# Optimization experiments

Hardware: AMD Instinct MI355X
Metric: run time of the kernel (lower is better)

The kernel has to match this reference:

```python
import jax, jax.numpy as jnp
import numpy as np

OBS, ACT, HID, P, B = 128, 32, 256, 64, 4096
EPS = 1e-5


def _block(x, W, b, g, be, act=True):
    # x: [B, P, Din]; W: [P, Din, Dout]; b/g/be: [P, Dout]
    y = jnp.einsum('bpi,pio->bpo', x, W) + b
    # GroupNorm with one group per sub-policy: normalize over Dout per (b, p)
    mu = jnp.mean(y, axis=-1, keepdims=True)
    var = jnp.var(y, axis=-1, keepdims=True)
    y = (y - mu) * jax.lax.rsqrt(var + EPS) * g + be
    return jax.nn.elu(y) if act else y


def setup_inputs() -> dict:
    key = jax.random.key(0)
    ks = jax.random.split(key, 17)
    s = 0.05
    return {
        'observation': jax.random.normal(ks[0], (B, OBS), dtype=jnp.float32),
        'W1': jax.random.normal(ks[1], (P, OBS, HID), dtype=jnp.float32) * s,
        'b1': jax.random.normal(ks[2], (P, HID), dtype=jnp.float32) * s,
        'g1': jnp.ones((P, HID), dtype=jnp.float32),
        'be1': jnp.zeros((P, HID), dtype=jnp.float32),
        'W2': jax.random.normal(ks[3], (P, HID, HID), dtype=jnp.float32) * s,
        'b2': jax.random.normal(ks[4], (P, HID), dtype=jnp.float32) * s,
        'g2': jnp.ones((P, HID), dtype=jnp.float32),
        'be2': jnp.zeros((P, HID), dtype=jnp.float32),
        'W3': jax.random.normal(ks[5], (P, HID, HID), dtype=jnp.float32) * s,
        'b3': jax.random.normal(ks[6], (P, HID), dtype=jnp.float32) * s,
        'g3': jnp.ones((P, HID), dtype=jnp.float32),
        'be3': jnp.zeros((P, HID), dtype=jnp.float32),
        'W4': jax.random.normal(ks[7], (P, HID, ACT), dtype=jnp.float32) * s,
        'b4': jax.random.normal(ks[8], (P, ACT), dtype=jnp.float32) * s,
        'g4': jnp.ones((P, ACT), dtype=jnp.float32),
        'be4': jnp.zeros((P, ACT), dtype=jnp.float32),
    }


def reference(observation, W1, b1, g1, be1, W2, b2, g2, be2,
              W3, b3, g3, be3, W4, b4, g4, be4):
    # broadcast observation to each sub-policy: [B, P, OBS]
    x = jnp.broadcast_to(observation[:, None, :], (observation.shape[0], P, OBS))
    x = _block(x, W1, b1, g1, be1, act=True)
    x = _block(x, W2, b2, g2, be2, act=True)
    x = _block(x, W3, b3, g3, be3, act=True)
    x = _block(x, W4, b4, g4, be4, act=False)
    return x  # [B, P, ACT] action logits
```

## Files before the change

### kernel.cpp

```cpp
#include <hip/hip_runtime.h>

#define B_    4096
#define P_    64
#define OBS_  128
#define HID_  256
#define ACTD_ 32

typedef __attribute__((ext_vector_type(8)))  __bf16 bf16x8;
typedef __attribute__((ext_vector_type(2)))  __bf16 bf16x2_t;
typedef __attribute__((ext_vector_type(4)))  float  f32x4;
typedef __attribute__((ext_vector_type(16))) float  f32x16;

#define XSTRIDE 264

#define WS1 0L
#define WS2 2097152L
#define WS3 6291456L
#define WS4 10485760L

#if defined(__has_builtin)
#if __has_builtin(__builtin_amdgcn_cvt_pk_bf16_f32)
#define HAVE_CVT_PK_BF16 1
#endif
#endif
#ifndef HAVE_CVT_PK_BF16
#define HAVE_CVT_PK_BF16 0
#endif

__device__ __forceinline__ unsigned short f2bf(float x) {
    unsigned u = __builtin_bit_cast(unsigned, x);
    u = (u + 0x7fffu + ((u >> 16) & 1u)) >> 16;
    return (unsigned short)u;
}

__device__ __forceinline__ unsigned pack_bf16_rne(float a, float b) {
#if HAVE_CVT_PK_BF16
    bf16x2_t p = __builtin_amdgcn_cvt_pk_bf16_f32(a, b);
    return __builtin_bit_cast(unsigned, p);
#else
    unsigned ua = __builtin_bit_cast(unsigned, a);
    unsigned ub = __builtin_bit_cast(unsigned, b);
    ua = ua + 0x7fffu + ((ua >> 16) & 1u);
    ub = ub + 0x7fffu + ((ub >> 16) & 1u);
    return __builtin_amdgcn_perm(ub, ua, 0x07060302u);
#endif
}

__device__ __forceinline__ float elu_asm(float v) {
    float r;
    asm volatile(
        "v_mul_f32 %0, 0x3fb8aa3b, %1\n\t"
        "v_exp_f32 %0, %0\n\t"
        "s_nop 1\n\t"
        "v_add_f32 %0, -1.0, %0\n\t"
        "v_cmp_lt_f32 vcc, 0, %1\n\t"
        "v_cndmask_b32 %0, %0, %1, vcc"
        : "=&v"(r) : "v"(v) : "vcc");
    return r;
}

template<int K, int N, bool PERM>
__device__ __forceinline__ void prep_body(const float* __restrict__ W,
                                          unsigned short* __restrict__ out,
                                          int b, int t)
{
    constexpr int CH = K / 32;
    int tid  = b * 256 + t;
    int n    = tid % N;
    int rest = tid / N;
    int u    = rest % 4;
    rest    /= 4;
    int c    = rest % CH;
    int p    = rest / CH;
    unsigned short tmp[8];
#pragma unroll
    for (int j = 0; j < 8; ++j) {
        int sk = c * 32 + u * 8 + j;
        int k  = PERM ? ((sk & ~63) | ((sk & 1) << 5) | ((sk >> 1) & 31)) : sk;
        tmp[j] = f2bf(W[((long)(p * K + k)) * N + n]);
    }
    unsigned short* dst = out + ((((long)(p * CH + c) * 4 + u) * N + n) * 8);
    *reinterpret_cast<uint4*>(dst) = *reinterpret_cast<const uint4*>(tmp);
}

extern "C" __global__ __launch_bounds__(256)
void prep_all(const float* __restrict__ W1, const float* __restrict__ W2,
              const float* __restrict__ W3, const float* __restrict__ W4,
              unsigned short* __restrict__ ws)
{
    int b = blockIdx.x, t = threadIdx.x;
    if      (b < 1024) prep_body<128, 256, false>(W1, ws + WS1, b,        t);
    else if (b < 3072) prep_body<256, 256, true >(W2, ws + WS2, b - 1024, t);
    else if (b < 5120) prep_body<256, 256, true >(W3, ws + WS3, b - 3072, t);
    else               prep_body<256, 32,  true >(W4, ws + WS4, b - 5120, t);
}

__device__ __forceinline__ void stage(char* lds, const char* src, int nbytes, int tid)
{
    const int lnoff = (tid & 63) * 16;
    const int off   = (tid >> 6) * 1024 + lnoff;
    for (int i = off; i < nbytes; i += 4096) {
        __builtin_amdgcn_global_load_lds(
            (const __attribute__((address_space(1))) unsigned int*)(const void*)(src + i),
            (__attribute__((address_space(3))) unsigned int*)(void*)(lds + (i - lnoff)),
            16, 0, 0);
    }
}

template<int KCH>
__device__ __forceinline__ void layer256(
    unsigned short* __restrict__ X,
    char* __restrict__ Wb0, char* __restrict__ Wb1,
    const char* __restrict__ wsrc,
    const char* __restrict__ nsrc, int nbytes,
    const float* __restrict__ bp, const float* __restrict__ gp, const float* __restrict__ bep,
    float2* __restrict__ part, float2* __restrict__ stats,
    int tid, bool elu)
{
    const int w  = tid >> 6;
    const int l5 = tid & 31;
    const int h  = (tid & 63) >> 5;

    f32x16 acc[2][2];
#pragma unroll
    for (int rt = 0; rt < 2; ++rt)
#pragma unroll
        for (int ct = 0; ct < 2; ++ct)
#pragma unroll
            for (int r = 0; r < 16; ++r) acc[rt][ct][r] = 0.f;

#pragma unroll
    for (int c = 0; c < KCH; ++c) {
        const char* nx = (c + 1 < KCH) ? (wsrc + (long)(c + 1) * 8192) : nsrc;
        int nb         = (c + 1 < KCH) ? 8192 : nbytes;
        stage((c & 1) ? Wb0 : Wb1, nx, nb, tid);

        const char* wc = (c & 1) ? Wb1 : Wb0;
        const int k0 = c * 16 + h * 8;
        bf16x8 a0 = *(const bf16x8*)(X + l5 * XSTRIDE + k0);
        bf16x8 a1 = *(const bf16x8*)(X + (32 + l5) * XSTRIDE + k0);
        const char* bb = wc + h * 4096;
        bf16x8 b0 = *(const bf16x8*)(bb + (w * 64 + l5) * 16);
        bf16x8 b1 = *(const bf16x8*)(bb + (w * 64 + 32 + l5) * 16);
        acc[0][0] = __builtin_amdgcn_mfma_f32_32x32x16_bf16(a0, b0, acc[0][0], 0, 0, 0);
        acc[1][0] = __builtin_amdgcn_mfma_f32_32x32x16_bf16(a1, b0, acc[1][0], 0, 0, 0);
        acc[0][1] = __builtin_amdgcn_mfma_f32_32x32x16_bf16(a0, b1, acc[0][1], 0, 0, 0);
        acc[1][1] = __builtin_amdgcn_mfma_f32_32x32x16_bf16(a1, b1, acc[1][1], 0, 0, 0);
        __syncthreads();
    }

    const int n0 = w * 64 + l5, n1 = n0 + 32;
    const int pos = w * 64 + 2 * l5;
    const float bb0 = bp[n0], bb1 = bp[n1];
#pragma unroll
    for (int rt = 0; rt < 2; ++rt)
#pragma unroll
        for (int r = 0; r < 16; ++r) { acc[rt][0][r] += bb0; acc[rt][1][r] += bb1; }

#pragma unroll
    for (int rt = 0; rt < 2; ++rt)
#pragma unroll
        for (int r = 0; r < 16; ++r) {
            const int row = rt * 32 + (r & 3) + 8 * (r >> 2) + 4 * h;
            *reinterpret_cast<unsigned*>(X + row * XSTRIDE + pos) =
                pack_bf16_rne(acc[rt][0][r], acc[rt][1][r]);
        }

    {
        const int lane = tid & 63;
        float s = 0.f, s2 = 0.f;
#pragma unroll
        for (int j8 = 0; j8 < 8; ++j8) {
            bf16x8 v8 = *(const bf16x8*)(X + lane * XSTRIDE + w * 64 + j8 * 8);
#pragma unroll
            for (int e = 0; e < 8; ++e) { float v = (float)v8[e]; s += v; s2 = fmaf(v, v, s2); }
        }
        part[lane * 4 + w] = make_float2(s, s2);
    }
    __syncthreads();
    if (w == 0) {
        const int lane = tid & 63;
        float2 p0 = part[lane * 4 + 0], p1 = part[lane * 4 + 1];
        float2 p2 = part[lane * 4 + 2], p3 = part[lane * 4 + 3];
        float s  = p0.x + p1.x + p2.x + p3.x;
        float s2 = p0.y + p1.y + p2.y + p3.y;
        float mu  = s * (1.f / 256.f);
        float var = s2 * (1.f / 256.f) - mu * mu;
        stats[lane] = make_float2(mu, rsqrtf(var + 1e-5f));
    }
    __syncthreads();

    const float g0 = gp[n0], g1 = gp[n1], be0 = bep[n0], be1 = bep[n1];
#pragma unroll
    for (int rt = 0; rt < 2; ++rt)
#pragma unroll
        for (int r = 0; r < 16; ++r) {
            const int row = rt * 32 + (r & 3) + 8 * (r >> 2) + 4 * h;
            float2 st = stats[row];
            float v0 = (acc[rt][0][r] - st.x) * st.y * g0 + be0;
            float v1 = (acc[rt][1][r] - st.x) * st.y * g1 + be1;
            if (elu) { v0 = elu_asm(v0); v1 = elu_asm(v1); }
            *reinterpret_cast<unsigned*>(X + row * XSTRIDE + pos) = pack_bf16_rne(v0, v1);
        }
    __syncthreads();
}

__device__ __forceinline__ void layer32(
    const unsigned short* __restrict__ X,
    char* __restrict__ Wb0, char* __restrict__ Wb1,
    const char* __restrict__ wsrc,
    const float* __restrict__ bp, const float* __restrict__ gp, const float* __restrict__ bep,
    float* __restrict__ outg, int bbase, int p, int tid)
{
    const int w = tid >> 6, lane = tid & 63, ln = lane & 15, quad = lane >> 4;
    f32x4 acc[2];
#pragma unroll
    for (int nt = 0; nt < 2; ++nt)
#pragma unroll
        for (int r = 0; r < 4; ++r) acc[nt][r] = 0.f;

#pragma unroll
    for (int c = 0; c < 8; ++c) {
        if (c < 7) stage((c & 1) ? Wb0 : Wb1, wsrc + (long)(c + 1) * 2048, 2048, tid);
        const char* wc = (c & 1) ? Wb1 : Wb0;
        bf16x8 a  = *(const bf16x8*)(X + (16 * w + ln) * XSTRIDE + c * 32 + quad * 8);
        bf16x8 b0 = *(const bf16x8*)(wc + quad * 512 + ln * 16);
        bf16x8 b1 = *(const bf16x8*)(wc + quad * 512 + (16 + ln) * 16);
        acc[0] = __builtin_amdgcn_mfma_f32_16x16x32_bf16(a, b0, acc[0], 0, 0, 0);
        acc[1] = __builtin_amdgcn_mfma_f32_16x16x32_bf16(a, b1, acc[1], 0, 0, 0);
        __syncthreads();
    }

    const float bb0 = bp[ln], bb1 = bp[16 + ln];
    const float g0 = gp[ln], g1 = gp[16 + ln], be0 = bep[ln], be1 = bep[16 + ln];
#pragma unroll
    for (int r = 0; r < 4; ++r) {
        float y0 = acc[0][r] + bb0, y1 = acc[1][r] + bb1;
        float s = y0 + y1, s2 = y0 * y0 + y1 * y1;
        s += __shfl_xor(s, 1);  s2 += __shfl_xor(s2, 1);
        s += __shfl_xor(s, 2);  s2 += __shfl_xor(s2, 2);
        s += __shfl_xor(s, 4);  s2 += __shfl_xor(s2, 4);
        s += __shfl_xor(s, 8);  s2 += __shfl_xor(s2, 8);
        float mu  = s * (1.f / 32.f);
        float var = s2 * (1.f / 32.f) - mu * mu;
        float rs  = rsqrtf(var + 1e-5f);
        const int row = bbase + 16 * w + quad * 4 + r;
        float* o = outg + ((long)row * P_ + p) * ACTD_;
        o[ln]      = (y0 - mu) * rs * g0 + be0;
        o[16 + ln] = (y1 - mu) * rs * g1 + be1;
    }
}

extern "C" __global__ void __launch_bounds__(256, 3)
policy_fused(const float* __restrict__ obs,
             const unsigned short* __restrict__ wbf,
             const float* __restrict__ b1, const float* __restrict__ g1, const float* __restrict__ be1,
             const float* __restrict__ b2, const float* __restrict__ g2, const float* __restrict__ be2,
             const float* __restrict__ b3, const float* __restrict__ g3, const float* __restrict__ be3,
             const float* __restrict__ b4, const float* __restrict__ g4, const float* __restrict__ be4,
             float* __restrict__ out)
{
    __shared__ __align__(16) unsigned short X[64 * XSTRIDE];
    __shared__ __align__(16) char Wbuf0[8192];
    __shared__ __align__(16) char Wbuf1[8192];
    __shared__ float2 part[64 * 4];
    __shared__ float2 stats[64];

    const int tid = threadIdx.x;
    const int bx  = blockIdx.x;
    const int p     = ((bx & 7) << 3) | ((bx >> 3) & 7);
    const int bbase = (bx >> 6) * 64;

    const char* ws1 = (const char*)(wbf + WS1 + (long)p * (128 * 256));
    const char* ws2 = (const char*)(wbf + WS2 + (long)p * (256 * 256));
    const char* ws3 = (const char*)(wbf + WS3 + (long)p * (256 * 256));
    const char* ws4 = (const char*)(wbf + WS4 + (long)p * (256 * 32));

    stage(Wbuf0, ws1, 8192, tid);

    for (int idx = tid; idx < 64 * 32; idx += 256) {
        int row = idx >> 5, c4 = idx & 31;
        float4 v = *reinterpret_cast<const float4*>(obs + (long)(bbase + row) * OBS_ + c4 * 4);
        uint2 pk;
        pk.x = pack_bf16_rne(v.x, v.y);
        pk.y = pack_bf16_rne(v.z, v.w);
        *reinterpret_cast<uint2*>(X + row * XSTRIDE + c4 * 4) = pk;
    }
    __syncthreads();

    layer256<8>(X, Wbuf0, Wbuf1, ws1, ws2, 8192,
                b1 + p * 256, g1 + p * 256, be1 + p * 256, part, stats, tid, true);
    layer256<16>(X, Wbuf0, Wbuf1, ws2, ws3, 8192,
                 b2 + p * 256, g2 + p * 256, be2 + p * 256, part, stats, tid, true);
    layer256<16>(X, Wbuf0, Wbuf1, ws3, ws4, 2048,
                 b3 + p * 256, g3 + p * 256, be3 + p * 256, part, stats, tid, true);
    layer32(X, Wbuf0, Wbuf1, ws4,
            b4 + p * 32, g4 + p * 32, be4 + p * 32, out, bbase, p, tid);
}

extern "C" void kernel_launch(void* const* d_in, const int* in_sizes, int n_in,
                              void* d_out, int out_size, void* d_ws, size_t ws_size,
                              hipStream_t stream)
{
    const float* obs = (const float*)d_in[0];
    const float* W1  = (const float*)d_in[1];
    const float* b1  = (const float*)d_in[2];
    const float* g1  = (const float*)d_in[3];
    const float* be1 = (const float*)d_in[4];
    const float* W2  = (const float*)d_in[5];
    const float* b2  = (const float*)d_in[6];
    const float* g2  = (const float*)d_in[7];
    const float* be2 = (const float*)d_in[8];
    const float* W3  = (const float*)d_in[9];
    const float* b3  = (const float*)d_in[10];
    const float* g3  = (const float*)d_in[11];
    const float* be3 = (const float*)d_in[12];
    const float* W4  = (const float*)d_in[13];
    const float* b4  = (const float*)d_in[14];
    const float* g4  = (const float*)d_in[15];
    const float* be4 = (const float*)d_in[16];
    float* out = (float*)d_out;
    unsigned short* ws = (unsigned short*)d_ws;

    hipLaunchKernelGGL(prep_all, dim3(5376), dim3(256), 0, stream, W1, W2, W3, W4, ws);

    hipLaunchKernelGGL(policy_fused, dim3(4096), dim3(256), 0, stream,
                       obs, ws,
                       b1, g1, be1, b2, g2, be2, b3, g3, be3, b4, g4, be4, out);
}
```

Before: 314.2 us.

## Load weight fragments directly from global memory instead of LDS double-buffering

Removes the LDS staging of weight chunks via global_load_lds with double buffers and per-chunk barriers. Each lane now reads its bf16 weight fragments straight from global (L2-cached) memory inside the fully unrolled K loop. This frees 16KB of LDS per block and drops many __syncthreads, which allows the occupancy hint to rise from 3 to 4 blocks per CU. The cost is that every wave fetches weights from global memory without LDS sharing, so performance now depends on L2 hit rates and on how well the compiler schedules loads ahead of the MFMAs.

```diff
diff --git a/kernel.cpp b/kernel.cpp
--- a/kernel.cpp
+++ b/kernel.cpp
@@ -95,24 +95,10 @@
     else               prep_body<256, 32,  true >(W4, ws + WS4, b - 5120, t);
 }
 
-__device__ __forceinline__ void stage(char* lds, const char* src, int nbytes, int tid)
-{
-    const int lnoff = (tid & 63) * 16;
-    const int off   = (tid >> 6) * 1024 + lnoff;
-    for (int i = off; i < nbytes; i += 4096) {
-        __builtin_amdgcn_global_load_lds(
-            (const __attribute__((address_space(1))) unsigned int*)(const void*)(src + i),
-            (__attribute__((address_space(3))) unsigned int*)(void*)(lds + (i - lnoff)),
-            16, 0, 0);
-    }
-}
-
 template<int KCH>
 __device__ __forceinline__ void layer256(
     unsigned short* __restrict__ X,
-    char* __restrict__ Wb0, char* __restrict__ Wb1,
     const char* __restrict__ wsrc,
-    const char* __restrict__ nsrc, int nbytes,
     const float* __restrict__ bp, const float* __restrict__ gp, const float* __restrict__ bep,
     float2* __restrict__ part, float2* __restrict__ stats,
     int tid, bool elu)
@@ -121,6 +107,8 @@
     const int l5 = tid & 31;
     const int h  = (tid & 63) >> 5;
 
+    const bf16x8* __restrict__ Bp = (const bf16x8*)wsrc + (h * 256 + w * 64 + l5);
+
     f32x16 acc[2][2];
 #pragma unroll
     for (int rt = 0; rt < 2; ++rt)
@@ -131,23 +119,17 @@
 
 #pragma unroll
     for (int c = 0; c < KCH; ++c) {
-        const char* nx = (c + 1 < KCH) ? (wsrc + (long)(c + 1) * 8192) : nsrc;
-        int nb         = (c + 1 < KCH) ? 8192 : nbytes;
-        stage((c & 1) ? Wb0 : Wb1, nx, nb, tid);
-
-        const char* wc = (c & 1) ? Wb1 : Wb0;
         const int k0 = c * 16 + h * 8;
         bf16x8 a0 = *(const bf16x8*)(X + l5 * XSTRIDE + k0);
         bf16x8 a1 = *(const bf16x8*)(X + (32 + l5) * XSTRIDE + k0);
-        const char* bb = wc + h * 4096;
-        bf16x8 b0 = *(const bf16x8*)(bb + (w * 64 + l5) * 16);
-        bf16x8 b1 = *(const bf16x8*)(bb + (w * 64 + 32 + l5) * 16);
+        bf16x8 b0 = Bp[c * 512];
+        bf16x8 b1 = Bp[c * 512 + 32];
         acc[0][0] = __builtin_amdgcn_mfma_f32_32x32x16_bf16(a0, b0, acc[0][0], 0, 0, 0);
         acc[1][0] = __builtin_amdgcn_mfma_f32_32x32x16_bf16(a1, b0, acc[1][0], 0, 0, 0);
         acc[0][1] = __builtin_amdgcn_mfma_f32_32x32x16_bf16(a0, b1, acc[0][1], 0, 0, 0);
         acc[1][1] = __builtin_amdgcn_mfma_f32_32x32x16_bf16(a1, b1, acc[1][1], 0, 0, 0);
-        __syncthreads();
-    }
+    }
+    __syncthreads();
 
     const int n0 = w * 64 + l5, n1 = n0 + 32;
     const int pos = w * 64 + 2 * l5;
@@ -207,12 +189,13 @@
 
 __device__ __forceinline__ void layer32(
     const unsigned short* __restrict__ X,
-    char* __restrict__ Wb0, char* __restrict__ Wb1,
     const char* __restrict__ wsrc,
     const float* __restrict__ bp, const float* __restrict__ gp, const float* __restrict__ bep,
     float* __restrict__ outg, int bbase, int p, int tid)
 {
     const int w = tid >> 6, lane = tid & 63, ln = lane & 15, quad = lane >> 4;
+    const bf16x8* __restrict__ Bp = (const bf16x8*)wsrc + (quad * 32 + ln);
+
     f32x4 acc[2];
 #pragma unroll
     for (int nt = 0; nt < 2; ++nt)
@@ -221,14 +204,11 @@
 
 #pragma unroll
     for (int c = 0; c < 8; ++c) {
-        if (c < 7) stage((c & 1) ? Wb0 : Wb1, wsrc + (long)(c + 1) * 2048, 2048, tid);
-        const char* wc = (c & 1) ? Wb1 : Wb0;
         bf16x8 a  = *(const bf16x8*)(X + (16 * w + ln) * XSTRIDE + c * 32 + quad * 8);
-        bf16x8 b0 = *(const bf16x8*)(wc + quad * 512 + ln * 16);
-        bf16x8 b1 = *(const bf16x8*)(wc + quad * 512 + (16 + ln) * 16);
+        bf16x8 b0 = Bp[c * 128];
+        bf16x8 b1 = Bp[c * 128 + 16];
         acc[0] = __builtin_amdgcn_mfma_f32_16x16x32_bf16(a, b0, acc[0], 0, 0, 0);
         acc[1] = __builtin_amdgcn_mfma_f32_16x16x32_bf16(a, b1, acc[1], 0, 0, 0);
-        __syncthreads();
     }
 
     const float bb0 = bp[ln], bb1 = bp[16 + ln];
@@ -251,7 +231,7 @@
     }
 }
 
-extern "C" __global__ void __launch_bounds__(256, 3)
+extern "C" __global__ void __launch_bounds__(256, 4)
 policy_fused(const float* __restrict__ obs,
              const unsigned short* __restrict__ wbf,
              const float* __restrict__ b1, const float* __restrict__ g1, const float* __restrict__ be1,
@@ -261,8 +241,6 @@
              float* __restrict__ out)
 {
     __shared__ __align__(16) unsigned short X[64 * XSTRIDE];
-    __shared__ __align__(16) char Wbuf0[8192];
-    __shared__ __align__(16) char Wbuf1[8192];
     __shared__ float2 part[64 * 4];
     __shared__ float2 stats[64];
 
@@ -275,8 +253,6 @@
     const char* ws2 = (const char*)(wbf + WS2 + (long)p * (256 * 256));
     const char* ws3 = (const char*)(wbf + WS3 + (long)p * (256 * 256));
     const char* ws4 = (const char*)(wbf + WS4 + (long)p * (256 * 32));
-
-    stage(Wbuf0, ws1, 8192, tid);
 
     for (int idx = tid; idx < 64 * 32; idx += 256) {
         int row = idx >> 5, c4 = idx & 31;
@@ -288,14 +264,10 @@
     }
     __syncthreads();
 
-    layer256<8>(X, Wbuf0, Wbuf1, ws1, ws2, 8192,
-                b1 + p * 256, g1 + p * 256, be1 + p * 256, part, stats, tid, true);
-    layer256<16>(X, Wbuf0, Wbuf1, ws2, ws3, 8192,
-                 b2 + p * 256, g2 + p * 256, be2 + p * 256, part, stats, tid, true);
-    layer256<16>(X, Wbuf0, Wbuf1, ws3, ws4, 2048,
-                 b3 + p * 256, g3 + p * 256, be3 + p * 256, part, stats, tid, true);
-    layer32(X, Wbuf0, Wbuf1, ws4,
-            b4 + p * 32, g4 + p * 32, be4 + p * 32, out, bbase, p, tid);
+    layer256<8>(X, ws1, b1 + p * 256, g1 + p * 256, be1 + p * 256, part, stats, tid, true);
+    layer256<16>(X, ws2, b2 + p * 256, g2 + p * 256, be2 + p * 256, part, stats, tid, true);
+    layer256<16>(X, ws3, b3 + p * 256, g3 + p * 256, be3 + p * 256, part, stats, tid, true);
+    layer32(X, ws4, b4 + p * 32, g4 + p * 32, be4 + p * 32, out, bbase, p, tid);
 }
 
 extern "C" void kernel_launch(void* const* d_in, const int* in_sizes, int n_in,
```

After: 283.2 us. 9.9% less time.
